# Performance work log

Hardware: AMD Instinct MI355X
Metric: run time of the kernel (lower is better)

The kernel has to match this reference:

```python
import jax, jax.numpy as jnp
import numpy as np

HEADS = 8
EPS = 1e-5

def _conv2d(x, w, b):
    # x: (b,c,h,w), w: (out_c,in_c,3,3), padding=1 (SAME)
    y = jax.lax.conv_general_dilated(x, w, (1, 1), ((1, 1), (1, 1)),
                                     dimension_numbers=('NCHW', 'OIHW', 'NCHW'))
    return y + b[None, :, None, None]

def _mcl(x, cw, cb, pw):
    # MultichannelLinear: conv then per-channel pointwise matmul over the h (feature) dim
    y = _conv2d(x, cw, cb)                      # (b,c,in_f,w)
    return jnp.einsum('bchw,cfh->bcfw', y, pw)  # (b,c,out_f,w)

def _ln(x, g, b):
    # MultichannelLayerNorm over the feature (h) axis with per-channel affine
    mu = x.mean(axis=2, keepdims=True)
    var = x.var(axis=2, keepdims=True)
    xn = (x - mu) * jax.lax.rsqrt(var + EPS)
    return xn * g[None, :, :, None] + b[None, :, :, None]

def _rope(t):
    # lucidrains RotaryEmbedding.rotate_queries_or_keys, interleaved pairs; t: (...,w,d)
    d = t.shape[-1]
    w = t.shape[-2]
    inv = 1.0 / (10000.0 ** (jnp.arange(0, d, 2, dtype=jnp.float32) / d))
    ang = jnp.arange(w, dtype=jnp.float32)[:, None] * inv[None, :]   # (w, d/2)
    cos = jnp.repeat(jnp.cos(ang), 2, axis=-1)
    sin = jnp.repeat(jnp.sin(ang), 2, axis=-1)
    t2 = t.reshape(t.shape[:-1] + (d // 2, 2))
    rot = jnp.stack([-t2[..., 1], t2[..., 0]], axis=-1).reshape(t.shape)
    return t * cos + rot * sin

def _split_heads(y, nh):
    b, c, f, w = y.shape
    return y.transpose(0, 1, 3, 2).reshape(b, c, w, nh, f // nh).transpose(0, 1, 3, 2, 4)  # (b,c,nh,w,dh)

def _forward(x, embed_cw, embed_cb, embed_pw, norm1_g, norm1_b,
             q_cw, q_cb, q_pw, k_cw, k_cb, k_pw, v_cw, v_cb, v_pw,
             o_cw, o_cb, o_pw, norm2_g, norm2_b,
             ffn1_cw, ffn1_cb, ffn1_pw, ffn2_cw, ffn2_cb, ffn2_pw):
    b, c_in, hdim, w = x.shape
    h0 = _mcl(x, embed_cw, embed_cb, embed_pw)          # (b,c,feat,w)
    # --- multichannel multihead attention with inline RoPE ---
    xn = _ln(h0, norm1_g, norm1_b)
    q = _rope(_split_heads(_mcl(xn, q_cw, q_cb, q_pw), HEADS))   # (b,c,nh,w,dh)
    k = _rope(_split_heads(_mcl(xn, k_cw, k_cb, k_pw), HEADS))
    v = _split_heads(_mcl(xn, v_cw, v_cb, v_pw), HEADS)
    qk = jnp.einsum('bchqd,bchkd->bchqk', q, k) / jnp.sqrt(jnp.float32(hdim))  # scale by sqrt(h), per source
    a = jnp.einsum('bchqk,bchkd->bchqd', jax.nn.softmax(qk, axis=-1), v)
    bb, cc, nh, ww, dh = a.shape
    a = a.transpose(0, 1, 3, 2, 4).reshape(bb, cc, ww, nh * dh).transpose(0, 1, 3, 2)  # (b,c,feat,w)
    z = _mcl(a, o_cw, o_cb, o_pw)
    h = h0 + z
    # --- squared-ReLU FFN ---
    y = _mcl(_ln(h, norm2_g, norm2_b), ffn1_cw, ffn1_cb, ffn1_pw)
    y = jnp.maximum(y, 0.0) ** 2
    z = _mcl(y, ffn2_cw, ffn2_cb, ffn2_pw)
    h = h + z
    return jnp.concatenate([x, h], axis=1)  # (b, c_in+c_out, feat, w)

def setup_inputs() -> dict:
    key = jax.random.key(0)
    ks = jax.random.split(key, 32)
    C_IN, C, F, W, B, EXP = 8, 4, 1024, 512, 4, 4

    def p(k, shape, fan):
        return jax.random.normal(k, shape, dtype=jnp.float32) * (1.0 / np.sqrt(fan))

    inp = {
        'x': jax.random.normal(ks[0], (B, C_IN, F, W), dtype=jnp.float32),
        'embed_cw': p(ks[1], (C, C_IN, 3, 3), C_IN * 9), 'embed_cb': p(ks[2], (C,), C_IN * 9),
        'embed_pw': p(ks[3], (C, F, F), F),
        'norm1_g': jnp.ones((C, F), jnp.float32), 'norm1_b': jnp.zeros((C, F), jnp.float32),
        'q_cw': p(ks[4], (C, C, 3, 3), C * 9), 'q_cb': p(ks[5], (C,), C * 9), 'q_pw': p(ks[6], (C, F, F), F),
        'k_cw': p(ks[7], (C, C, 3, 3), C * 9), 'k_cb': p(ks[8], (C,), C * 9), 'k_pw': p(ks[9], (C, F, F), F),
        'v_cw': p(ks[10], (C, C, 3, 3), C * 9), 'v_cb': p(ks[11], (C,), C * 9), 'v_pw': p(ks[12], (C, F, F), F),
        'o_cw': p(ks[13], (C, C, 3, 3), C * 9), 'o_cb': p(ks[14], (C,), C * 9), 'o_pw': p(ks[15], (C, F, F), F),
        'norm2_g': jnp.ones((C, F), jnp.float32), 'norm2_b': jnp.zeros((C, F), jnp.float32),
        'ffn1_cw': p(ks[16], (C, C, 3, 3), C * 9), 'ffn1_cb': p(ks[17], (C,), C * 9),
        'ffn1_pw': p(ks[18], (C, F * EXP, F), F),
        'ffn2_cw': p(ks[19], (C, C, 3, 3), C * 9), 'ffn2_cb': p(ks[20], (C,), C * 9),
        'ffn2_pw': p(ks[21], (C, F, F * EXP), F * EXP),
    }
    return inp

def reference(x, embed_cw, embed_cb, embed_pw, norm1_g, norm1_b,
              q_cw, q_cb, q_pw, k_cw, k_cb, k_pw, v_cw, v_cb, v_pw,
              o_cw, o_cb, o_pw, norm2_g, norm2_b,
              ffn1_cw, ffn1_cb, ffn1_pw, ffn2_cw, ffn2_cb, ffn2_pw):
    return _forward(x, embed_cw, embed_cb, embed_pw, norm1_g, norm1_b,
                    q_cw, q_cb, q_pw, k_cw, k_cb, k_pw, v_cw, v_cb, v_pw,
                    o_cw, o_cb, o_pw, norm2_g, norm2_b,
                    ffn1_cw, ffn1_cb, ffn1_pw, ffn2_cw, ffn2_cb, ffn2_pw)
```

## Files before the change

### kernel.cpp

```cpp
#include <hip/hip_runtime.h>

typedef __attribute__((ext_vector_type(8))) short short8;
typedef __attribute__((ext_vector_type(4))) float f32x4;
typedef unsigned int uint;
typedef unsigned short ushort;

#define PLF 524288

__device__ __forceinline__ ushort f2bf(float f) {
  uint u = __float_as_uint(f);
  u += 0x7FFF + ((u >> 16) & 1);
  return (ushort)(u >> 16);
}
__device__ __forceinline__ float bf2f(ushort h) {
  return __uint_as_float(((uint)h) << 16);
}
__device__ __forceinline__ int swzf(int r) { return ((r & 3) ^ ((r >> 2) & 3)); }

#define GLOAD16(gp, lp)                                          \
  __builtin_amdgcn_global_load_lds(                              \
      (const __attribute__((address_space(1))) void*)(gp),       \
      (__attribute__((address_space(3))) void*)(lp), 16, 0, 0)

template <int CDT, int BETA, int RELU2, int MFAST, int BCVT, int ROPE>
__global__ __launch_bounds__(256) void mm_kernel(
    const void* __restrict__ Av, const void* __restrict__ Bv, void* __restrict__ Cv,
    int K, int lda, int ldb, int ldc,
    int aDiv, int aMod, long long aS1, long long aS2,
    int bDiv, int bMod, long long bS1, long long bS2,
    int cDiv, int cMod, long long cS1, long long cS2, float alpha)
{
  __shared__ char lds[49152];
  const int nx = gridDim.x, ny = gridDim.y;
  const int nwg = nx * ny * (int)gridDim.z;
  const int o = ((int)blockIdx.z * ny + blockIdx.y) * nx + blockIdx.x;
  const int qd = nwg >> 3, rm = nwg & 7, xcd = o & 7, rot = o >> 3;
  const int wflat = (xcd < rm ? xcd * (qd + 1) : rm * (qd + 1) + (xcd - rm) * qd) + rot;
  int bx, by, bz;
  if (MFAST) { by = wflat % ny; int t2 = wflat / ny; bx = t2 % nx; bz = t2 / nx; }
  else       { bx = wflat % nx; int t2 = wflat / nx; by = t2 % ny; bz = t2 / ny; }
  const int tid = threadIdx.x;
  const long long aOff = (long long)(bz / aDiv) * aS1 + (long long)(bz % aMod) * aS2;
  const long long bOff = (long long)(bz / bDiv) * bS1 + (long long)(bz % bMod) * bS2;
  const long long cOff = (long long)(bz / cDiv) * cS1 + (long long)(bz % cMod) * cS2;
  const int m0 = by * 128, n0 = bx * 128;
  const int lane = tid & 63, wid = tid >> 6;
  const int MOFF = (wid >> 1) * 64, NOFF = (wid & 1) * 64;
  const int u = lane & 15, g = lane >> 4;
  const int sr0 = tid >> 2, sslot = tid & 3;
  const ushort* Ap = (const ushort*)Av + aOff;
  const ushort* Bp = (const ushort*)Bv + bOff;
  const float*  Bf = (const float*)Bv + bOff;

#define STAGE(buf, kt)                                                         \
  {                                                                            \
    _Pragma("unroll")                                                          \
    for (int half = 0; half < 2; ++half) {                                     \
      const int r = sr0 + 64 * half;                                           \
      const int ss = sslot ^ swzf(r);                                          \
      GLOAD16(Ap + (long long)(m0 + r) * lda + (kt) + ss * 8,                  \
              &lds[(buf) * 16384] + wid * 1024 + half * 4096);                 \
      if (BCVT == 0) {                                                         \
        GLOAD16(Bp + (long long)(n0 + r) * ldb + (kt) + ss * 8,                \
                &lds[(buf) * 16384 + 8192] + wid * 1024 + half * 4096);        \
      } else {                                                                 \
        const float* srcB = Bf + (long long)(n0 + r) * ldb + (kt) + ss * 8;    \
        float4 x0 = *(const float4*)srcB;                                      \
        float4 x1 = *(const float4*)(srcB + 4);                                \
        short8 h;                                                              \
        h[0] = (short)f2bf(x0.x); h[1] = (short)f2bf(x0.y);                    \
        h[2] = (short)f2bf(x0.z); h[3] = (short)f2bf(x0.w);                    \
        h[4] = (short)f2bf(x1.x); h[5] = (short)f2bf(x1.y);                    \
        h[6] = (short)f2bf(x1.z); h[7] = (short)f2bf(x1.w);                    \
        *(short8*)(&lds[(buf) * 16384 + 8192] + r * 64 + sslot * 16) = h;      \
      }                                                                        \
    }                                                                          \
  }

  f32x4 acc[4][4];
#pragma unroll
  for (int i = 0; i < 4; ++i)
#pragma unroll
    for (int j = 0; j < 4; ++j) acc[i][j] = (f32x4){0.f, 0.f, 0.f, 0.f};

  const int T = K >> 5;
  STAGE(0, 0);
  if (T > 1) STAGE(1, 32);
  int rb = 0, sb = 2;
  for (int t = 0; t < T; ++t) {
    if (BCVT == 0) {
      if (t + 1 < T) { asm volatile("s_waitcnt vmcnt(4)" ::: "memory"); }
      else           { asm volatile("s_waitcnt vmcnt(0)" ::: "memory"); }
    } else {
      asm volatile("s_waitcnt vmcnt(0) lgkmcnt(0)" ::: "memory");
    }
    __builtin_amdgcn_s_barrier();
    __builtin_amdgcn_sched_barrier(0);
    asm volatile("" ::: "memory");
    if (t + 2 < T) STAGE(sb, (t + 2) * 32);
    const char* Abuf = &lds[rb * 16384];
    const char* Bbuf = &lds[rb * 16384 + 8192];
    short8 af[4], bfr[4];
#pragma unroll
    for (int mi = 0; mi < 4; ++mi) {
      const int r = MOFF + mi * 16 + u;
      af[mi] = *(const short8*)(Abuf + r * 64 + ((g ^ swzf(r)) * 16));
    }
#pragma unroll
    for (int ni = 0; ni < 4; ++ni) {
      const int r = NOFF + ni * 16 + u;
      bfr[ni] = *(const short8*)(Bbuf + r * 64 + ((g ^ swzf(r)) * 16));
    }
#pragma unroll
    for (int mi = 0; mi < 4; ++mi)
#pragma unroll
      for (int ni = 0; ni < 4; ++ni)
        acc[mi][ni] = __builtin_amdgcn_mfma_f32_16x16x32_bf16(af[mi], bfr[ni], acc[mi][ni], 0, 0, 0);
    rb = (rb == 2) ? 0 : rb + 1;
    sb = (sb == 2) ? 0 : sb + 1;
  }
#undef STAGE

#pragma unroll
  for (int mi = 0; mi < 4; ++mi)
#pragma unroll
    for (int ni = 0; ni < 4; ++ni)
#pragma unroll
      for (int q = 0; q < 4; ++q) {
        const int row = m0 + MOFF + mi * 16 + g * 4 + q;
        const int col = n0 + NOFF + ni * 16 + u;
        float v = acc[mi][ni][q] * alpha;
        if (CDT == 0) {
          float* cp = (float*)Cv + cOff + (long long)row * ldc + col;
          if (BETA) v += *cp;
          *cp = v;
        } else {
          if (ROPE) {
            const int j = (col & 127) >> 1;
            const float infr = __expf((float)j * (-9.210340371976184f / 64.f));
            float sn, cs;
            __sincosf((float)row * infr, &sn, &cs);
            const float part = __shfl_xor(v, 1);
            v = (col & 1) ? fmaf(part, sn, v * cs) : fmaf(-part, sn, v * cs);
          }
          if (RELU2) { v = fmaxf(v, 0.f); v = v * v; }
          ((ushort*)Cv)[cOff + (long long)row * ldc + col] = f2bf(v);
        }
      }
}

__global__ __launch_bounds__(256) void fattn_kernel(
    const ushort* __restrict__ Qg, const ushort* __restrict__ Kg,
    const ushort* __restrict__ Vg, ushort* __restrict__ Og)
{
  __shared__ char lds[73728];
  const int hb = blockIdx.y, pl = hb >> 3, h = hb & 7;
  const int q0 = blockIdx.x * 64;
  const int tid = threadIdx.x, lane = tid & 63, wv = tid >> 6;
  const int u = lane & 15, g = lane >> 4;
  const ushort* Qh = Qg + (size_t)pl * PLF + h * 128;
  const ushort* Kh = Kg + (size_t)pl * PLF + h * 128;
  const ushort* Vh = Vg + (size_t)pl * PLF + (size_t)(h * 128) * 512;
  ushort* Oh = Og + (size_t)pl * PLF + h * 128;

  short8 qf[4];
  const int qrow = q0 + wv * 16 + u;
#pragma unroll
  for (int dc = 0; dc < 4; ++dc)
    qf[dc] = *(const short8*)(Qh + (size_t)qrow * 1024 + dc * 32 + g * 8);

#define STAGE_KV(buf, kt)                                                     \
  {                                                                           \
    _Pragma("unroll")                                                         \
    for (int it = 0; it < 4; ++it) {                                          \
      const int off = tid * 16 + it * 4096;                                   \
      const int krow = off >> 8, kslot = (off >> 4) & 15;                     \
      GLOAD16(Kh + (size_t)((kt) * 64 + krow) * 1024 +                        \
                  ((kslot ^ ((krow & 7) << 1)) * 8),                          \
              &lds[(buf) * 16384] + off);                                     \
      const int vrow = off >> 7, vslot = (off >> 4) & 7;                      \
      GLOAD16(Vh + (size_t)vrow * 512 + (kt) * 64 + ((vslot ^ (vrow & 7)) * 8), \
              &lds[32768 + (buf) * 16384] + off);                             \
    }                                                                         \
  }

  f32x4 oacc[8];
#pragma unroll
  for (int i = 0; i < 8; ++i) oacc[i] = (f32x4){0.f, 0.f, 0.f, 0.f};
  float m_run = -3.0e38f, l_run = 0.f;

  STAGE_KV(0, 0);
  asm volatile("s_waitcnt vmcnt(0)" ::: "memory");
  __syncthreads();
  int cur = 0;
  for (int kt = 0; kt < 8; ++kt) {
    if (kt + 1 < 8) STAGE_KV(cur ^ 1, kt + 1);
    f32x4 sacc[4];
#pragma unroll
    for (int kn = 0; kn < 4; ++kn) sacc[kn] = (f32x4){0.f, 0.f, 0.f, 0.f};
#pragma unroll
    for (int kn = 0; kn < 4; ++kn) {
      const int r = kn * 16 + u;
      const char* kb = &lds[cur * 16384] + r * 256;
#pragma unroll
      for (int dc = 0; dc < 4; ++dc) {
        short8 kf = *(const short8*)(kb + (((dc * 4 + g) ^ ((u & 7) << 1)) * 16));
        sacc[kn] = __builtin_amdgcn_mfma_f32_16x16x32_bf16(kf, qf[dc], sacc[kn], 0, 0, 0);
      }
    }
    float pm = -3.0e38f;
#pragma unroll
    for (int kn = 0; kn < 4; ++kn)
#pragma unroll
      for (int r = 0; r < 4; ++r) {
        sacc[kn][r] *= 0.03125f;
        pm = fmaxf(pm, sacc[kn][r]);
      }
    pm = fmaxf(pm, __shfl_xor(pm, 16));
    pm = fmaxf(pm, __shfl_xor(pm, 32));
    const float m_new = fmaxf(m_run, pm);
    const float es = __expf(m_run - m_new);
    float psum = 0.f;
    uint pw[4][2];
#pragma unroll
    for (int kn = 0; kn < 4; ++kn) {
      float p0 = __expf(sacc[kn][0] - m_new);
      float p1 = __expf(sacc[kn][1] - m_new);
      float p2 = __expf(sacc[kn][2] - m_new);
      float p3 = __expf(sacc[kn][3] - m_new);
      psum += (p0 + p1) + (p2 + p3);
      pw[kn][0] = (uint)f2bf(p0) | ((uint)f2bf(p1) << 16);
      pw[kn][1] = (uint)f2bf(p2) | ((uint)f2bf(p3) << 16);
    }
    psum += __shfl_xor(psum, 16);
    psum += __shfl_xor(psum, 32);
    l_run = l_run * es + psum;
    m_run = m_new;
    char* pb = &lds[65536 + wv * 2048] + u * 128 + (g & 1) * 8;
#pragma unroll
    for (int kn = 0; kn < 4; ++kn)
      *(uint2*)(pb + (((2 * kn + (g >> 1)) ^ (u & 7)) * 16)) =
          make_uint2(pw[kn][0], pw[kn][1]);
    float es_o[4];
#pragma unroll
    for (int r = 0; r < 4; ++r) es_o[r] = __shfl(es, g * 4 + r);
#pragma unroll
    for (int nd = 0; nd < 8; ++nd)
#pragma unroll
      for (int r = 0; r < 4; ++r) oacc[nd][r] *= es_o[r];
    const char* prd = &lds[65536 + wv * 2048] + u * 128;
    short8 pf[2];
#pragma unroll
    for (int kc = 0; kc < 2; ++kc)
      pf[kc] = *(const short8*)(prd + (((kc * 4 + g) ^ (u & 7)) * 16));
#pragma unroll
    for (int nd = 0; nd < 8; ++nd) {
      const int vr = nd * 16 + u;
      const char* vb = &lds[32768 + cur * 16384] + vr * 128;
#pragma unroll
      for (int kc = 0; kc < 2; ++kc) {
        short8 vf = *(const short8*)(vb + (((kc * 4 + g) ^ (u & 7)) * 16));
        oacc[nd] = __builtin_amdgcn_mfma_f32_16x16x32_bf16(pf[kc], vf, oacc[nd], 0, 0, 0);
      }
    }
    asm volatile("s_waitcnt vmcnt(0)" ::: "memory");
    __syncthreads();
    cur ^= 1;
  }
#undef STAGE_KV
  const float inv_l = 1.f / l_run;
  float inv_o[4];
#pragma unroll
  for (int r = 0; r < 4; ++r) inv_o[r] = __shfl(inv_l, g * 4 + r);
#pragma unroll
  for (int nd = 0; nd < 8; ++nd)
#pragma unroll
    for (int r = 0; r < 4; ++r) {
      const int row = q0 + wv * 16 + g * 4 + r;
      Oh[(size_t)row * 1024 + nd * 16 + u] = f2bf(oacc[nd][r] * inv_o[r]);
    }
}

__global__ __launch_bounds__(256) void cvt_kernel(
    const float4* __restrict__ s, short8* __restrict__ d)
{
  const int i = blockIdx.x * 256 + threadIdx.x;
  const float4 a = s[2 * i], b = s[2 * i + 1];
  short8 h;
  h[0] = (short)f2bf(a.x); h[1] = (short)f2bf(a.y);
  h[2] = (short)f2bf(a.z); h[3] = (short)f2bf(a.w);
  h[4] = (short)f2bf(b.x); h[5] = (short)f2bf(b.y);
  h[6] = (short)f2bf(b.z); h[7] = (short)f2bf(b.w);
  d[i] = h;
}

template <int CIN>
__global__ __launch_bounds__(256) void conv4c_kernel(
    const ushort* __restrict__ in, const float* __restrict__ wt,
    const float* __restrict__ bias, ushort* __restrict__ outp, int log2F)
{
  const int idx = blockIdx.x * 256 + threadIdx.x;
  const int F8m = (1 << (log2F - 3)) - 1;
  const int f8 = idx & F8m;
  const int w = (idx >> (log2F - 3)) & 511;
  const int bb = idx >> (log2F + 6);
  const int f0 = f8 << 3;
  float acc[4][8];
#pragma unroll
  for (int co = 0; co < 4; ++co) {
    const float bv = bias[co];
#pragma unroll
    for (int j = 0; j < 8; ++j) acc[co][j] = bv;
  }
  const bool lok = f8 > 0, rok = f8 < F8m;
#pragma unroll
  for (int ci = 0; ci < CIN; ++ci) {
    const ushort* base = in + (((size_t)(bb * CIN + ci)) << (log2F + 9));
#pragma unroll
    for (int dxw = 0; dxw < 3; ++dxw) {
      const int w2 = w + dxw - 1;
      if (w2 < 0 || w2 > 511) continue;
      const ushort* rp = base + ((size_t)w2 << log2F) + f0;
      const short8 cen = *(const short8*)rp;
      float xv[10];
      xv[0] = lok ? bf2f(rp[-1]) : 0.f;
#pragma unroll
      for (int j = 0; j < 8; ++j) xv[j + 1] = bf2f((ushort)cen[j]);
      xv[9] = rok ? bf2f(rp[8]) : 0.f;
#pragma unroll
      for (int co = 0; co < 4; ++co) {
        const float* wp = wt + (co * CIN + ci) * 9;
        const float k0 = wp[dxw], k1 = wp[3 + dxw], k2 = wp[6 + dxw];
#pragma unroll
        for (int j = 0; j < 8; ++j)
          acc[co][j] += k0 * xv[j] + k1 * xv[j + 1] + k2 * xv[j + 2];
      }
    }
  }
#pragma unroll
  for (int co = 0; co < 4; ++co) {
    short8 o;
#pragma unroll
    for (int j = 0; j < 8; ++j) o[j] = (short)f2bf(acc[co][j]);
    *(short8*)(outp + (((size_t)(bb * 4 + co)) << (log2F + 9)) + ((size_t)w << log2F) + f0) = o;
  }
}

__global__ __launch_bounds__(256) void conv12c_kernel(
    const ushort* __restrict__ in,
    const float* __restrict__ wq, const float* __restrict__ wk, const float* __restrict__ wv,
    const float* __restrict__ bq, const float* __restrict__ bk, const float* __restrict__ bv,
    ushort* __restrict__ outp, int nPl)
{
  const int idx = blockIdx.x * 256 + threadIdx.x;
  const int f8 = idx & 127;
  const int w = (idx >> 7) & 511;
  const int bb = idx >> 16;
  const int f0 = f8 << 3;
  const float* wsel[3] = {wq, wk, wv};
  float acc[12][8];
#pragma unroll
  for (int co = 0; co < 4; ++co) {
    const float b0 = bq[co], b1 = bk[co], b2 = bv[co];
#pragma unroll
    for (int j = 0; j < 8; ++j) {
      acc[co][j] = b0; acc[4 + co][j] = b1; acc[8 + co][j] = b2;
    }
  }
  const bool lok = f8 > 0, rok = f8 < 127;
#pragma unroll
  for (int ci = 0; ci < 4; ++ci) {
    const ushort* base = in + (((size_t)(bb * 4 + ci)) << 19);
#pragma unroll
    for (int dxw = 0; dxw < 3; ++dxw) {
      const int w2 = w + dxw - 1;
      if (w2 < 0 || w2 > 511) continue;
      const ushort* rp = base + ((size_t)w2 << 10) + f0;
      const short8 cen = *(const short8*)rp;
      float xv[10];
      xv[0] = lok ? bf2f(rp[-1]) : 0.f;
#pragma unroll
      for (int j = 0; j < 8; ++j) xv[j + 1] = bf2f((ushort)cen[j]);
      xv[9] = rok ? bf2f(rp[8]) : 0.f;
#pragma unroll
      for (int pj = 0; pj < 3; ++pj)
#pragma unroll
        for (int co = 0; co < 4; ++co) {
          const float* wp = wsel[pj] + (co * 4 + ci) * 9;
          const float k0 = wp[dxw], k1 = wp[3 + dxw], k2 = wp[6 + dxw];
#pragma unroll
          for (int j = 0; j < 8; ++j)
            acc[pj * 4 + co][j] += k0 * xv[j] + k1 * xv[j + 1] + k2 * xv[j + 2];
        }
    }
  }
#pragma unroll
  for (int pj = 0; pj < 3; ++pj)
#pragma unroll
    for (int co = 0; co < 4; ++co) {
      short8 o;
#pragma unroll
      for (int j = 0; j < 8; ++j) o[j] = (short)f2bf(acc[pj * 4 + co][j]);
      *(short8*)(outp + (((size_t)(pj * nPl + bb * 4 + co)) << 19) +
                 ((size_t)w << 10) + f0) = o;
    }
}

__global__ __launch_bounds__(256) void ln_kernel(
    const float* __restrict__ H, const float* __restrict__ gam,
    const float* __restrict__ bet, ushort* __restrict__ XN)
{
  const int wid = threadIdx.x >> 6, lane = threadIdx.x & 63;
  const int row = blockIdx.x * 4 + wid;
  const int c = (row >> 9) & 3;
  const float* xp = H + (size_t)row * 1024;
  float4 v[4];
  float s = 0.f, q = 0.f;
#pragma unroll
  for (int p = 0; p < 4; ++p) {
    v[p] = *(const float4*)(xp + p * 256 + lane * 4);
    s += v[p].x + v[p].y + v[p].z + v[p].w;
    q += v[p].x * v[p].x + v[p].y * v[p].y + v[p].z * v[p].z + v[p].w * v[p].w;
  }
#pragma unroll
  for (int o = 32; o > 0; o >>= 1) { s += __shfl_xor(s, o); q += __shfl_xor(q, o); }
  const float mu = s * (1.f / 1024.f);
  const float var = q * (1.f / 1024.f) - mu * mu;
  const float rs = rsqrtf(var + 1e-5f);
  ushort* op = XN + (size_t)row * 1024;
  const float* gp = gam + c * 1024;
  const float* bp = bet + c * 1024;
#pragma unroll
  for (int p = 0; p < 4; ++p) {
    const int f = p * 256 + lane * 4;
    float4 g4 = *(const float4*)(gp + f);
    float4 b4 = *(const float4*)(bp + f);
    ushort4 o4;
    o4.x = f2bf((v[p].x - mu) * rs * g4.x + b4.x);
    o4.y = f2bf((v[p].y - mu) * rs * g4.y + b4.y);
    o4.z = f2bf((v[p].z - mu) * rs * g4.z + b4.z);
    o4.w = f2bf((v[p].w - mu) * rs * g4.w + b4.w);
    *(ushort4*)(op + f) = o4;
  }
}

__global__ __launch_bounds__(256) void tin_kernel(
    const float* __restrict__ x, ushort* __restrict__ XT,
    float* __restrict__ outp, int planeOff)
{
  __shared__ float t[32][33];
  const int f0 = blockIdx.x * 32, w0 = blockIdx.y * 32;
  const int z = blockIdx.z;
  const int tx = threadIdx.x & 31, ty = threadIdx.x >> 5;
  const int gpl = planeOff + z;
  const int b = gpl >> 3, ch = gpl & 7;
  const float* src = x + (size_t)gpl * PLF;
  float* dst0 = outp + (size_t)(b * 12 + ch) * PLF;
#pragma unroll
  for (int r = 0; r < 32; r += 8) {
    const size_t off = (size_t)(f0 + r + ty) * 512 + w0 + tx;
    const float v = src[off];
    t[r + ty][tx] = v;
    dst0[off] = v;
  }
  __syncthreads();
  ushort* dst = XT + (size_t)z * PLF;
#pragma unroll
  for (int r = 0; r < 32; r += 8) dst[(size_t)(w0 + r + ty) * 1024 + f0 + tx] = f2bf(t[tx][r + ty]);
}

__global__ __launch_bounds__(256) void tout_kernel(
    const float* __restrict__ H, float* __restrict__ out, int b0)
{
  __shared__ float t[32][33];
  const int w0 = blockIdx.x * 32, f0 = blockIdx.y * 32;
  const int p = blockIdx.z;
  const int b = b0 + (p >> 2), c = p & 3;
  const int tx = threadIdx.x & 31, ty = threadIdx.x >> 5;
  const float* src = H + (size_t)p * PLF;
#pragma unroll
  for (int r = 0; r < 32; r += 8) t[r + ty][tx] = src[(size_t)(w0 + r + ty) * 1024 + f0 + tx];
  __syncthreads();
  float* dst = out + (size_t)(b * 12 + 8 + c) * PLF;
#pragma unroll
  for (int r = 0; r < 32; r += 8) dst[(size_t)(f0 + r + ty) * 512 + w0 + tx] = t[tx][r + ty];
}

extern "C" void kernel_launch(void* const* d_in, const int* in_sizes, int n_in,
                              void* d_out, int out_size, void* d_ws, size_t ws_size,
                              hipStream_t stream)
{
  const float* x        = (const float*)d_in[0];
  const float* embed_cw = (const float*)d_in[1];
  const float* embed_cb = (const float*)d_in[2];
  const float* embed_pw = (const float*)d_in[3];
  const float* n1g      = (const float*)d_in[4];
  const float* n1b      = (const float*)d_in[5];
  const float* q_cw     = (const float*)d_in[6];
  const float* q_cb     = (const float*)d_in[7];
  const float* q_pw     = (const float*)d_in[8];
  const float* k_cw     = (const float*)d_in[9];
  const float* k_cb     = (const float*)d_in[10];
  const float* k_pw     = (const float*)d_in[11];
  const float* v_cw     = (const float*)d_in[12];
  const float* v_cb     = (const float*)d_in[13];
  const float* v_pw     = (const float*)d_in[14];
  const float* o_cw     = (const float*)d_in[15];
  const float* o_cb     = (const float*)d_in[16];
  const float* o_pw     = (const float*)d_in[17];
  const float* n2g      = (const float*)d_in[18];
  const float* n2b      = (const float*)d_in[19];
  const float* f1_cw    = (const float*)d_in[20];
  const float* f1_cb    = (const float*)d_in[21];
  const float* f1_pw    = (const float*)d_in[22];
  const float* f2_cw    = (const float*)d_in[23];
  const float* f2_cb    = (const float*)d_in[24];
  const float* f2_pw    = (const float*)d_in[25];
  float* out = (float*)d_out;

  const size_t perB = 50331648ull;
  const int N = (ws_size >= 4 * perB) ? 4 : (ws_size >= 2 * perB) ? 2 : 1;
  const int nP = 4 * N;

  char* base = (char*)d_ws;
  float*  Hf = (float*)base;
  ushort* XT = (ushort*)(base + (size_t)N * 8388608);
  ushort* XN = (ushort*)((char*)XT + (size_t)N * 8388608);
  ushort* Qb = (ushort*)((char*)XN + (size_t)N * 4194304);
  ushort* Kb = (ushort*)((char*)Qb + (size_t)N * 4194304);
  ushort* CT = (ushort*)((char*)Kb + (size_t)N * 4194304);
  ushort* Vb = (ushort*)((char*)CT + (size_t)N * 4194304);
  ushort* SfPb = (ushort*)((char*)Vb + (size_t)N * 4194304);
  ushort* CT3 = SfPb;
  ushort* W8  = SfPb;
  ushort* WQK = XT;
  ushort* MID = XT;
  ushort* f1w = Vb;
  ushort* F2C = Vb;
  ushort* f2w = XT;

  const long long W1 = 1048576;
  const long long W4 = 4194304;
  const long long M1 = 2097152;
  const long long CH3 = (long long)nP * PLF;
  const int GCc1 = N * 256;
  const int GCc4 = N * 1024;

  for (int b0 = 0; b0 < 4; b0 += N) {
    tin_kernel<<<dim3(32, 16, 8 * N), 256, 0, stream>>>(x, XT, out, b0 * 8);
    conv4c_kernel<8><<<GCc1, 256, 0, stream>>>(XT, embed_cw, embed_cb, CT, 10);
    cvt_kernel<<<2048, 256, 0, stream>>>((const float4*)embed_pw, (short8*)W8);
    mm_kernel<0, 0, 0, 0, 0, 0><<<dim3(8, 4, nP), 256, 0, stream>>>(
        CT, W8, Hf, 1024, 1024, 1024, 1024,
        1, 1, PLF, 0, 4, 4, 0, W1, 1, 1, PLF, 0, 1.f);
    ln_kernel<<<nP * 128, 256, 0, stream>>>(Hf, n1g, n1b, XN);
    conv12c_kernel<<<GCc1, 256, 0, stream>>>(XN, q_cw, k_cw, v_cw,
                                             q_cb, k_cb, v_cb, CT3, nP);
    if (N >= 2) {
      cvt_kernel<<<2048, 256, 0, stream>>>((const float4*)q_pw, (short8*)WQK);
      cvt_kernel<<<2048, 256, 0, stream>>>((const float4*)k_pw, (short8*)(WQK) + 524288);
      mm_kernel<1, 0, 0, 0, 0, 1><<<dim3(8, 4, 2 * nP), 256, 0, stream>>>(
          CT3, WQK, Qb, 1024, 1024, 1024, 1024,
          1, 1, PLF, 0, nP, 4, 4 * W1, W1, 1, 1, PLF, 0, 1.f);
    } else {
      mm_kernel<1, 0, 0, 0, 1, 1><<<dim3(8, 4, nP), 256, 0, stream>>>(
          CT3, q_pw, Qb, 1024, 1024, 1024, 1024,
          1, 1, PLF, 0, 4, 4, 0, W1, 1, 1, PLF, 0, 1.f);
      mm_kernel<1, 0, 0, 0, 1, 1><<<dim3(8, 4, nP), 256, 0, stream>>>(
          CT3 + CH3, k_pw, Kb, 1024, 1024, 1024, 1024,
          1, 1, PLF, 0, 4, 4, 0, W1, 1, 1, PLF, 0, 1.f);
    }
    cvt_kernel<<<2048, 256, 0, stream>>>((const float4*)v_pw, (short8*)W8);
    mm_kernel<1, 0, 0, 0, 0, 0><<<dim3(4, 8, nP), 256, 0, stream>>>(
        W8, CT3 + 2 * CH3, Vb, 1024, 1024, 1024, 512,
        4, 4, 0, W1, 1, 1, PLF, 0, 1, 1, PLF, 0, 1.f);
    fattn_kernel<<<dim3(8, nP * 8), 256, 0, stream>>>(Qb, Kb, Vb, Qb);
    conv4c_kernel<4><<<GCc1, 256, 0, stream>>>(Qb, o_cw, o_cb, CT, 10);
    cvt_kernel<<<2048, 256, 0, stream>>>((const float4*)o_pw, (short8*)W8);
    mm_kernel<0, 1, 0, 0, 0, 0><<<dim3(8, 4, nP), 256, 0, stream>>>(
        CT, W8, Hf, 1024, 1024, 1024, 1024,
        1, 1, PLF, 0, 4, 4, 0, W1, 1, 1, PLF, 0, 1.f);
    ln_kernel<<<nP * 128, 256, 0, stream>>>(Hf, n2g, n2b, XN);
    conv4c_kernel<4><<<GCc1, 256, 0, stream>>>(XN, f1_cw, f1_cb, CT, 10);
    if (N >= 2) {
      cvt_kernel<<<8192, 256, 0, stream>>>((const float4*)f1_pw, (short8*)f1w);
      mm_kernel<1, 0, 1, 1, 0, 0><<<dim3(32, 4, nP), 256, 0, stream>>>(
          CT, f1w, MID, 1024, 1024, 1024, 4096,
          1, 1, PLF, 0, 4, 4, 0, W4, 1, 1, M1, 0, 1.f);
    } else {
      mm_kernel<1, 0, 1, 1, 1, 0><<<dim3(32, 4, nP), 256, 0, stream>>>(
          CT, f1_pw, MID, 1024, 1024, 1024, 4096,
          1, 1, PLF, 0, 4, 4, 0, W4, 1, 1, M1, 0, 1.f);
    }
    conv4c_kernel<4><<<GCc4, 256, 0, stream>>>(MID, f2_cw, f2_cb, F2C, 12);
    if (N >= 2) {
      cvt_kernel<<<8192, 256, 0, stream>>>((const float4*)f2_pw, (short8*)f2w);
      mm_kernel<0, 1, 0, 0, 0, 0><<<dim3(8, 4, nP), 256, 0, stream>>>(
          F2C, f2w, Hf, 4096, 4096, 4096, 1024,
          1, 1, M1, 0, 4, 4, 0, W4, 1, 1, PLF, 0, 1.f);
    } else {
      mm_kernel<0, 1, 0, 0, 1, 0><<<dim3(8, 4, nP), 256, 0, stream>>>(
          F2C, f2_pw, Hf, 4096, 4096, 4096, 1024,
          1, 1, M1, 0, 4, 4, 0, W4, 1, 1, PLF, 0, 1.f);
    }
    tout_kernel<<<dim3(16, 32, nP), 256, 0, stream>>>(Hf, out, b0);
  }
}
```

Measured before the change: 651.1 us.

## Add split-K with atomic accumulation for residual GEMMs and MFMA priority hints

Adds a split-K template parameter to the GEMM kernel. The output projection and the FFN2 GEMMs, which accumulate into the residual buffer, now launch twice as many workgroups, each covering half of K, and combine partial sums with float atomicAdd in place of read-modify-write. The intent is to fill more compute units on these launches, which have low workgroup counts. Separately, s_setprio raises wave priority around the MFMA blocks in both the GEMM and the flash-attention kernel. Atomics make the summation order nondeterministic and add memory contention in exchange.

```diff
diff --git a/kernel.cpp b/kernel.cpp
--- a/kernel.cpp
+++ b/kernel.cpp
@@ -22,7 +22,7 @@
       (const __attribute__((address_space(1))) void*)(gp),       \
       (__attribute__((address_space(3))) void*)(lp), 16, 0, 0)
 
-template <int CDT, int BETA, int RELU2, int MFAST, int BCVT, int ROPE>
+template <int CDT, int BETA, int RELU2, int MFAST, int BCVT, int ROPE, int KS>
 __global__ __launch_bounds__(256) void mm_kernel(
     const void* __restrict__ Av, const void* __restrict__ Bv, void* __restrict__ Cv,
     int K, int lda, int ldb, int ldc,
@@ -39,6 +39,9 @@
   int bx, by, bz;
   if (MFAST) { by = wflat % ny; int t2 = wflat / ny; bx = t2 % nx; bz = t2 / nx; }
   else       { bx = wflat % nx; int t2 = wflat / nx; by = t2 % ny; bz = t2 / ny; }
+  int kb = 0;
+  if (KS > 1) { kb = (bz % KS) * (K / KS); bz /= KS; }
+  const int KH = K / KS;
   const int tid = threadIdx.x;
   const long long aOff = (long long)(bz / aDiv) * aS1 + (long long)(bz % aMod) * aS2;
   const long long bOff = (long long)(bz / bDiv) * bS1 + (long long)(bz % bMod) * bS2;
@@ -48,9 +51,9 @@
   const int MOFF = (wid >> 1) * 64, NOFF = (wid & 1) * 64;
   const int u = lane & 15, g = lane >> 4;
   const int sr0 = tid >> 2, sslot = tid & 3;
-  const ushort* Ap = (const ushort*)Av + aOff;
-  const ushort* Bp = (const ushort*)Bv + bOff;
-  const float*  Bf = (const float*)Bv + bOff;
+  const ushort* Ap = (const ushort*)Av + aOff + kb;
+  const ushort* Bp = (const ushort*)Bv + bOff + kb;
+  const float*  Bf = (const float*)Bv + bOff + kb;
 
 #define STAGE(buf, kt)                                                         \
   {                                                                            \
@@ -83,7 +86,7 @@
 #pragma unroll
     for (int j = 0; j < 4; ++j) acc[i][j] = (f32x4){0.f, 0.f, 0.f, 0.f};
 
-  const int T = K >> 5;
+  const int T = KH >> 5;
   STAGE(0, 0);
   if (T > 1) STAGE(1, 32);
   int rb = 0, sb = 2;
@@ -111,11 +114,13 @@
       const int r = NOFF + ni * 16 + u;
       bfr[ni] = *(const short8*)(Bbuf + r * 64 + ((g ^ swzf(r)) * 16));
     }
+    __builtin_amdgcn_s_setprio(1);
 #pragma unroll
     for (int mi = 0; mi < 4; ++mi)
 #pragma unroll
       for (int ni = 0; ni < 4; ++ni)
         acc[mi][ni] = __builtin_amdgcn_mfma_f32_16x16x32_bf16(af[mi], bfr[ni], acc[mi][ni], 0, 0, 0);
+    __builtin_amdgcn_s_setprio(0);
     rb = (rb == 2) ? 0 : rb + 1;
     sb = (sb == 2) ? 0 : sb + 1;
   }
@@ -132,8 +137,12 @@
         float v = acc[mi][ni][q] * alpha;
         if (CDT == 0) {
           float* cp = (float*)Cv + cOff + (long long)row * ldc + col;
-          if (BETA) v += *cp;
-          *cp = v;
+          if (KS > 1) {
+            atomicAdd(cp, v);
+          } else {
+            if (BETA) v += *cp;
+            *cp = v;
+          }
         } else {
           if (ROPE) {
             const int j = (col & 127) >> 1;
@@ -198,6 +207,7 @@
     f32x4 sacc[4];
 #pragma unroll
     for (int kn = 0; kn < 4; ++kn) sacc[kn] = (f32x4){0.f, 0.f, 0.f, 0.f};
+    __builtin_amdgcn_s_setprio(1);
 #pragma unroll
     for (int kn = 0; kn < 4; ++kn) {
       const int r = kn * 16 + u;
@@ -208,6 +218,7 @@
         sacc[kn] = __builtin_amdgcn_mfma_f32_16x16x32_bf16(kf, qf[dc], sacc[kn], 0, 0, 0);
       }
     }
+    __builtin_amdgcn_s_setprio(0);
     float pm = -3.0e38f;
 #pragma unroll
     for (int kn = 0; kn < 4; ++kn)
@@ -253,6 +264,7 @@
 #pragma unroll
     for (int kc = 0; kc < 2; ++kc)
       pf[kc] = *(const short8*)(prd + (((kc * 4 + g) ^ (u & 7)) * 16));
+    __builtin_amdgcn_s_setprio(1);
 #pragma unroll
     for (int nd = 0; nd < 8; ++nd) {
       const int vr = nd * 16 + u;
@@ -263,6 +275,7 @@
         oacc[nd] = __builtin_amdgcn_mfma_f32_16x16x32_bf16(pf[kc], vf, oacc[nd], 0, 0, 0);
       }
     }
+    __builtin_amdgcn_s_setprio(0);
     asm volatile("s_waitcnt vmcnt(0)" ::: "memory");
     __syncthreads();
     cur ^= 1;
@@ -550,7 +563,7 @@
     tin_kernel<<<dim3(32, 16, 8 * N), 256, 0, stream>>>(x, XT, out, b0 * 8);
     conv4c_kernel<8><<<GCc1, 256, 0, stream>>>(XT, embed_cw, embed_cb, CT, 10);
     cvt_kernel<<<2048, 256, 0, stream>>>((const float4*)embed_pw, (short8*)W8);
-    mm_kernel<0, 0, 0, 0, 0, 0><<<dim3(8, 4, nP), 256, 0, stream>>>(
+    mm_kernel<0, 0, 0, 0, 0, 0, 1><<<dim3(8, 4, nP), 256, 0, stream>>>(
         CT, W8, Hf, 1024, 1024, 1024, 1024,
         1, 1, PLF, 0, 4, 4, 0, W1, 1, 1, PLF, 0, 1.f);
     ln_kernel<<<nP * 128, 256, 0, stream>>>(Hf, n1g, n1b, XN);
@@ -559,47 +572,47 @@
     if (N >= 2) {
       cvt_kernel<<<2048, 256, 0, stream>>>((const float4*)q_pw, (short8*)WQK);
       cvt_kernel<<<2048, 256, 0, stream>>>((const float4*)k_pw, (short8*)(WQK) + 524288);
-      mm_kernel<1, 0, 0, 0, 0, 1><<<dim3(8, 4, 2 * nP), 256, 0, stream>>>(
+      mm_kernel<1, 0, 0, 0, 0, 1, 1><<<dim3(8, 4, 2 * nP), 256, 0, stream>>>(
           CT3, WQK, Qb, 1024, 1024, 1024, 1024,
           1, 1, PLF, 0, nP, 4, 4 * W1, W1, 1, 1, PLF, 0, 1.f);
     } else {
-      mm_kernel<1, 0, 0, 0, 1, 1><<<dim3(8, 4, nP), 256, 0, stream>>>(
+      mm_kernel<1, 0, 0, 0, 1, 1, 1><<<dim3(8, 4, nP), 256, 0, stream>>>(
           CT3, q_pw, Qb, 1024, 1024, 1024, 1024,
           1, 1, PLF, 0, 4, 4, 0, W1, 1, 1, PLF, 0, 1.f);
-      mm_kernel<1, 0, 0, 0, 1, 1><<<dim3(8, 4, nP), 256, 0, stream>>>(
+      mm_kernel<1, 0, 0, 0, 1, 1, 1><<<dim3(8, 4, nP), 256, 0, stream>>>(
           CT3 + CH3, k_pw, Kb, 1024, 1024, 1024, 1024,
           1, 1, PLF, 0, 4, 4, 0, W1, 1, 1, PLF, 0, 1.f);
     }
     cvt_kernel<<<2048, 256, 0, stream>>>((const float4*)v_pw, (short8*)W8);
-    mm_kernel<1, 0, 0, 0, 0, 0><<<dim3(4, 8, nP), 256, 0, stream>>>(
+    mm_kernel<1, 0, 0, 0, 0, 0, 1><<<dim3(4, 8, nP), 256, 0, stream>>>(
         W8, CT3 + 2 * CH3, Vb, 1024, 1024, 1024, 512,
         4, 4, 0, W1, 1, 1, PLF, 0, 1, 1, PLF, 0, 1.f);
     fattn_kernel<<<dim3(8, nP * 8), 256, 0, stream>>>(Qb, Kb, Vb, Qb);
     conv4c_kernel<4><<<GCc1, 256, 0, stream>>>(Qb, o_cw, o_cb, CT, 10);
     cvt_kernel<<<2048, 256, 0, stream>>>((const float4*)o_pw, (short8*)W8);
-    mm_kernel<0, 1, 0, 0, 0, 0><<<dim3(8, 4, nP), 256, 0, stream>>>(
+    mm_kernel<0, 0, 0, 0, 0, 0, 2><<<dim3(8, 4, 2 * nP), 256, 0, stream>>>(
         CT, W8, Hf, 1024, 1024, 1024, 1024,
         1, 1, PLF, 0, 4, 4, 0, W1, 1, 1, PLF, 0, 1.f);
     ln_kernel<<<nP * 128, 256, 0, stream>>>(Hf, n2g, n2b, XN);
     conv4c_kernel<4><<<GCc1, 256, 0, stream>>>(XN, f1_cw, f1_cb, CT, 10);
     if (N >= 2) {
       cvt_kernel<<<8192, 256, 0, stream>>>((const float4*)f1_pw, (short8*)f1w);
-      mm_kernel<1, 0, 1, 1, 0, 0><<<dim3(32, 4, nP), 256, 0, stream>>>(
+      mm_kernel<1, 0, 1, 1, 0, 0, 1><<<dim3(32, 4, nP), 256, 0, stream>>>(
           CT, f1w, MID, 1024, 1024, 1024, 4096,
           1, 1, PLF, 0, 4, 4, 0, W4, 1, 1, M1, 0, 1.f);
     } else {
-      mm_kernel<1, 0, 1, 1, 1, 0><<<dim3(32, 4, nP), 256, 0, stream>>>(
+      mm_kernel<1, 0, 1, 1, 1, 0, 1><<<dim3(32, 4, nP), 256, 0, stream>>>(
           CT, f1_pw, MID, 1024, 1024, 1024, 4096,
           1, 1, PLF, 0, 4, 4, 0, W4, 1, 1, M1, 0, 1.f);
     }
     conv4c_kernel<4><<<GCc4, 256, 0, stream>>>(MID, f2_cw, f2_cb, F2C, 12);
     if (N >= 2) {
       cvt_kernel<<<8192, 256, 0, stream>>>((const float4*)f2_pw, (short8*)f2w);
-      mm_kernel<0, 1, 0, 0, 0, 0><<<dim3(8, 4, nP), 256, 0, stream>>>(
+      mm_kernel<0, 0, 0, 0, 0, 0, 2><<<dim3(8, 4, 2 * nP), 256, 0, stream>>>(
           F2C, f2w, Hf, 4096, 4096, 4096, 1024,
           1, 1, M1, 0, 4, 4, 0, W4, 1, 1, PLF, 0, 1.f);
     } else {
-      mm_kernel<0, 1, 0, 0, 1, 0><<<dim3(8, 4, nP), 256, 0, stream>>>(
+      mm_kernel<0, 1, 0, 0, 1, 0, 1><<<dim3(8, 4, nP), 256, 0, stream>>>(
           F2C, f2_pw, Hf, 4096, 4096, 4096, 1024,
           1, 1, M1, 0, 4, 4, 0, W4, 1, 1, PLF, 0, 1.f);
     }
```

After: 699.0 us. 1.07x slower.
